# Performance work log

Hardware: AMD Instinct MI355X
Metric: run time of the kernel (lower is better)

Reference implementation:

```python
import jax, jax.numpy as jnp
import numpy as np

TEMPERATURE = 0.1
EPS = 1e-12  # F.normalize default eps


def _l2norm(x):
    n = jnp.sqrt(jnp.sum(x * x, axis=-1, keepdims=True))
    return x / jnp.maximum(n, EPS)


def setup_inputs() -> dict:
    key = jax.random.key(0)
    k1, k2, k3 = jax.random.split(key, 3)
    G, NA, NO, D = 256, 256, 512, 128
    student_nodes = jax.random.normal(k1, (G * NA, D), dtype=jnp.float32)
    teacher_nodes = jax.random.normal(k2, (G * NO, D), dtype=jnp.float32)
    # local indices into each original graph's node block (as in t_nodes_all[kept_indices])
    kept_node_indices = jax.random.randint(k3, (G * NA,), 0, NO, dtype=jnp.int64)
    return {
        "student_nodes": student_nodes,
        "teacher_nodes": teacher_nodes,
        "kept_node_indices": kept_node_indices,
        "num_graphs": G,
        "n_aug": NA,
        "n_orig": NO,
    }


def reference(student_nodes, teacher_nodes, kept_node_indices, num_graphs, n_aug, n_orig):
    D = student_nodes.shape[-1]
    # ragged batch regularized: ptr boundaries -> fixed-size reshape
    s = _l2norm(student_nodes.reshape(num_graphs, n_aug, D))      # [G, Na, D]
    t = _l2norm(teacher_nodes.reshape(num_graphs, n_orig, D))     # [G, No, D]
    kept = kept_node_indices.reshape(num_graphs, n_aug)           # [G, Na]
    t_aligned = jnp.take_along_axis(t, kept[:, :, None], axis=1)  # [G, Na, D]
    scores = jnp.einsum("gid,gjd->gij", s, t_aligned) / TEMPERATURE  # [G, Na, Na]
    logp = jax.nn.log_softmax(scores, axis=-1)
    idx = jnp.arange(n_aug)
    # CE with labels = arange: -logp[g, i, i], mean over i per graph, then mean over graphs
    per_graph_ce = -jnp.mean(logp[:, idx, idx], axis=-1)          # [G]
    return jnp.mean(per_graph_ce)
```

## Files before the change

### kernel.cpp

```cpp
#include <hip/hip_runtime.h>
#include <hip/hip_bf16.h>

using f32x4  = __attribute__((ext_vector_type(4))) float;
using bf16x8 = __attribute__((ext_vector_type(8))) short;

constexpr int   G_NUM = 256;
constexpr int   NAUG  = 256;
constexpr int   NORIG = 512;
constexpr int   DIM   = 128;
constexpr float INV_T = 10.0f;

__device__ __forceinline__ short f32_to_bf16_bits(float x) {
    unsigned u = __float_as_uint(x);
    u += 0x7fffu + ((u >> 16) & 1u);
    return (short)(u >> 16);
}

__global__ __launch_bounds__(512, 4) void nlcl_main(
    const float* __restrict__ student,
    const float* __restrict__ teacher,
    const int*   __restrict__ kept,
    float*       __restrict__ block_sums)
{
    __shared__ short t_lds[NAUG * DIM];
    __shared__ float rt_lds[NAUG];
    __shared__ float rs_lds[128];
    __shared__ float red[8];

    const int bid = blockIdx.x;
    const int logical = (bid & 7) * 64 + (bid >> 3);
    const int g    = logical >> 1;
    const int half = logical & 1;

    const int tid  = threadIdx.x;
    const int lane = tid & 63;
    const int wave = tid >> 6;
    const int rbase = half * 128;

    const float* s_base = student + (size_t)g * NAUG * DIM;
    const float* t_base = teacher + (size_t)g * NORIG * DIM;
    const int*   k_base = kept + g * NAUG;

    const int ccol  = lane & 15;
    const int cquad = lane >> 4;

    const int hw = tid >> 5;
    const int hl = tid & 31;

    int idxv[16];
    #pragma unroll
    for (int it = 0; it < 16; ++it) idxv[it] = k_base[it * 16 + hw];

    const int srow = rbase + wave * 16 + ccol;
    const float* rp = s_base + srow * DIM;
    float4 sv[8];
    #pragma unroll
    for (int kc = 0; kc < 4; ++kc) {
        sv[kc * 2]     = *reinterpret_cast<const float4*>(rp + kc * 32 + cquad * 8);
        sv[kc * 2 + 1] = *reinterpret_cast<const float4*>(rp + kc * 32 + cquad * 8 + 4);
    }

    float4 gv0[4], gv1[4];
    #pragma unroll
    for (int i = 0; i < 4; ++i)
        gv0[i] = *reinterpret_cast<const float4*>(t_base + (size_t)idxv[i] * DIM + hl * 4);
    #pragma unroll
    for (int i = 0; i < 4; ++i)
        gv1[i] = *reinterpret_cast<const float4*>(t_base + (size_t)idxv[4 + i] * DIM + hl * 4);

    bf16x8 afrag[4];
    {
        float ss = 0.f;
        #pragma unroll
        for (int kc = 0; kc < 4; ++kc) {
            const float4 a = sv[kc * 2], b = sv[kc * 2 + 1];
            afrag[kc][0] = f32_to_bf16_bits(a.x); afrag[kc][1] = f32_to_bf16_bits(a.y);
            afrag[kc][2] = f32_to_bf16_bits(a.z); afrag[kc][3] = f32_to_bf16_bits(a.w);
            afrag[kc][4] = f32_to_bf16_bits(b.x); afrag[kc][5] = f32_to_bf16_bits(b.y);
            afrag[kc][6] = f32_to_bf16_bits(b.z); afrag[kc][7] = f32_to_bf16_bits(b.w);
            ss += a.x * a.x + a.y * a.y + a.z * a.z + a.w * a.w;
            ss += b.x * b.x + b.y * b.y + b.z * b.z + b.w * b.w;
        }
        ss += __shfl_xor(ss, 16);
        ss += __shfl_xor(ss, 32);
        if (cquad == 0)
            rs_lds[wave * 16 + ccol] = rsqrtf(fmaxf(ss, 1e-24f)) * INV_T;
    }

    char* tl = reinterpret_cast<char*>(t_lds);
    #pragma unroll
    for (int c = 0; c < 4; ++c) {
        float4 cur[4];
        #pragma unroll
        for (int i = 0; i < 4; ++i) cur[i] = (c & 1) ? gv1[i] : gv0[i];
        if (c < 2) {
            #pragma unroll
            for (int i = 0; i < 4; ++i) {
                float4 nxt = *reinterpret_cast<const float4*>(
                    t_base + (size_t)idxv[(c + 2) * 4 + i] * DIM + hl * 4);
                if (c & 1) gv1[i] = nxt; else gv0[i] = nxt;
            }
        }
        #pragma unroll
        for (int i = 0; i < 4; ++i) {
            const int it = c * 4 + i;
            const int j  = it * 16 + hw;
            const float4 v = cur[i];
            short4 o;
            o.x = f32_to_bf16_bits(v.x); o.y = f32_to_bf16_bits(v.y);
            o.z = f32_to_bf16_bits(v.z); o.w = f32_to_bf16_bits(v.w);
            const int byte = j * 256 + ((hl * 8) ^ ((j & 7) << 4));
            *reinterpret_cast<short4*>(tl + byte) = o;
            float ss = v.x * v.x + v.y * v.y + v.z * v.z + v.w * v.w;
            ss += __shfl_xor(ss, 1);
            ss += __shfl_xor(ss, 2);
            ss += __shfl_xor(ss, 4);
            ss += __shfl_xor(ss, 8);
            ss += __shfl_xor(ss, 16);
            if (hl == 0)
                rt_lds[j] = rsqrtf(fmaxf(ss, 1e-24f));
        }
    }
    __syncthreads();

    float sumexp[4] = {0.f, 0.f, 0.f, 0.f};
    float diagsum = 0.f;
    const char* tlc = reinterpret_cast<const char*>(t_lds);
    float rs[4];
    #pragma unroll
    for (int reg = 0; reg < 4; ++reg)
        rs[reg] = rs_lds[wave * 16 + cquad * 4 + reg];

    for (int ct = 0; ct < 16; ++ct) {
        f32x4 acc = {0.f, 0.f, 0.f, 0.f};
        const int j = ct * 16 + ccol;
        const float rt = rt_lds[j];
        #pragma unroll
        for (int kc = 0; kc < 4; ++kc) {
            const int byte = j * 256 + (((kc * 64) + (cquad * 16)) ^ ((j & 7) << 4));
            const bf16x8 b = *reinterpret_cast<const bf16x8*>(tlc + byte);
            acc = __builtin_amdgcn_mfma_f32_16x16x32_bf16(afrag[kc], b, acc, 0, 0, 0);
        }
        #pragma unroll
        for (int reg = 0; reg < 4; ++reg) {
            const int row = rbase + wave * 16 + cquad * 4 + reg;
            const float l = acc[reg] * rs[reg] * rt;
            sumexp[reg] += __expf(l);
            if (j == row) diagsum += l;
        }
    }

    float ce = 0.f;
    #pragma unroll
    for (int reg = 0; reg < 4; ++reg) {
        float s = sumexp[reg];
        s += __shfl_xor(s, 1);
        s += __shfl_xor(s, 2);
        s += __shfl_xor(s, 4);
        s += __shfl_xor(s, 8);
        if (ccol == 0) ce += __logf(s);
    }
    ce -= diagsum;
    ce += __shfl_xor(ce, 1);
    ce += __shfl_xor(ce, 2);
    ce += __shfl_xor(ce, 4);
    ce += __shfl_xor(ce, 8);
    ce += __shfl_xor(ce, 16);
    ce += __shfl_xor(ce, 32);

    if (lane == 0) red[wave] = ce;
    __syncthreads();
    if (tid == 0) {
        float t = 0.f;
        #pragma unroll
        for (int w = 0; w < 8; ++w) t += red[w];
        block_sums[bid] = t;
    }
}

__global__ void nlcl_reduce(const float* __restrict__ block_sums,
                            float* __restrict__ out)
{
    __shared__ float r[8];
    const int tid = threadIdx.x;
    float v = block_sums[tid];
    v += __shfl_xor(v, 1);
    v += __shfl_xor(v, 2);
    v += __shfl_xor(v, 4);
    v += __shfl_xor(v, 8);
    v += __shfl_xor(v, 16);
    v += __shfl_xor(v, 32);
    if ((tid & 63) == 0) r[tid >> 6] = v;
    __syncthreads();
    if (tid == 0) {
        float t = 0.f;
        #pragma unroll
        for (int w = 0; w < 8; ++w) t += r[w];
        out[0] = t * (1.0f / ((float)G_NUM * (float)NAUG));
    }
}

extern "C" void kernel_launch(void* const* d_in, const int* in_sizes, int n_in,
                              void* d_out, int out_size, void* d_ws, size_t ws_size,
                              hipStream_t stream) {
    (void)in_sizes; (void)n_in; (void)out_size; (void)ws_size;
    const float* student = (const float*)d_in[0];
    const float* teacher = (const float*)d_in[1];
    const int*   kept    = (const int*)d_in[2];
    float* bs  = (float*)d_ws;
    float* out = (float*)d_out;

    nlcl_main<<<512, 512, 0, stream>>>(student, teacher, kept, bs);
    nlcl_reduce<<<1, 512, 0, stream>>>(bs, out);
}
```

Measured before the change: 25.13 us.

## Split teacher staging into two halves and fuse final reduction via last-block atomic

Issues all sixteen teacher row gathers up front in two register batches, stores the first half to LDS, and syncs. It then overlaps storing the second half with MFMA over the first half, separated by a second barrier. The separate reduce kernel is replaced by a last-block-done atomic counter pattern, with the counter zeroed by a memset each call. This doubles the register footprint for gathered rows, which may reduce occupancy, and trades one kernel launch for a memset plus an atomic.

```diff
diff --git a/kernel.cpp b/kernel.cpp
--- a/kernel.cpp
+++ b/kernel.cpp
@@ -4,11 +4,12 @@
 using f32x4  = __attribute__((ext_vector_type(4))) float;
 using bf16x8 = __attribute__((ext_vector_type(8))) short;
 
-constexpr int   G_NUM = 256;
-constexpr int   NAUG  = 256;
-constexpr int   NORIG = 512;
-constexpr int   DIM   = 128;
-constexpr float INV_T = 10.0f;
+constexpr int   G_NUM  = 256;
+constexpr int   NAUG   = 256;
+constexpr int   NORIG  = 512;
+constexpr int   DIM    = 128;
+constexpr float INV_T  = 10.0f;
+constexpr int   NBLK   = 512;
 
 __device__ __forceinline__ short f32_to_bf16_bits(float x) {
     unsigned u = __float_as_uint(x);
@@ -20,12 +21,15 @@
     const float* __restrict__ student,
     const float* __restrict__ teacher,
     const int*   __restrict__ kept,
-    float*       __restrict__ block_sums)
+    float*       __restrict__ block_sums,
+    unsigned*    __restrict__ counter,
+    float*       __restrict__ out)
 {
     __shared__ short t_lds[NAUG * DIM];
     __shared__ float rt_lds[NAUG];
     __shared__ float rs_lds[128];
     __shared__ float red[8];
+    __shared__ int   is_last;
 
     const int bid = blockIdx.x;
     const int logical = (bid & 7) * 64 + (bid >> 3);
@@ -60,13 +64,13 @@
         sv[kc * 2 + 1] = *reinterpret_cast<const float4*>(rp + kc * 32 + cquad * 8 + 4);
     }
 
-    float4 gv0[4], gv1[4];
-    #pragma unroll
-    for (int i = 0; i < 4; ++i)
+    float4 gv0[8], gv1[8];
+    #pragma unroll
+    for (int i = 0; i < 8; ++i)
         gv0[i] = *reinterpret_cast<const float4*>(t_base + (size_t)idxv[i] * DIM + hl * 4);
     #pragma unroll
-    for (int i = 0; i < 4; ++i)
-        gv1[i] = *reinterpret_cast<const float4*>(t_base + (size_t)idxv[4 + i] * DIM + hl * 4);
+    for (int i = 0; i < 8; ++i)
+        gv1[i] = *reinterpret_cast<const float4*>(t_base + (size_t)idxv[8 + i] * DIM + hl * 4);
 
     bf16x8 afrag[4];
     {
@@ -89,39 +93,41 @@
 
     char* tl = reinterpret_cast<char*>(t_lds);
     #pragma unroll
-    for (int c = 0; c < 4; ++c) {
-        float4 cur[4];
-        #pragma unroll
-        for (int i = 0; i < 4; ++i) cur[i] = (c & 1) ? gv1[i] : gv0[i];
-        if (c < 2) {
-            #pragma unroll
-            for (int i = 0; i < 4; ++i) {
-                float4 nxt = *reinterpret_cast<const float4*>(
-                    t_base + (size_t)idxv[(c + 2) * 4 + i] * DIM + hl * 4);
-                if (c & 1) gv1[i] = nxt; else gv0[i] = nxt;
-            }
-        }
-        #pragma unroll
-        for (int i = 0; i < 4; ++i) {
-            const int it = c * 4 + i;
-            const int j  = it * 16 + hw;
-            const float4 v = cur[i];
-            short4 o;
-            o.x = f32_to_bf16_bits(v.x); o.y = f32_to_bf16_bits(v.y);
-            o.z = f32_to_bf16_bits(v.z); o.w = f32_to_bf16_bits(v.w);
-            const int byte = j * 256 + ((hl * 8) ^ ((j & 7) << 4));
-            *reinterpret_cast<short4*>(tl + byte) = o;
-            float ss = v.x * v.x + v.y * v.y + v.z * v.z + v.w * v.w;
-            ss += __shfl_xor(ss, 1);
-            ss += __shfl_xor(ss, 2);
-            ss += __shfl_xor(ss, 4);
-            ss += __shfl_xor(ss, 8);
-            ss += __shfl_xor(ss, 16);
-            if (hl == 0)
-                rt_lds[j] = rsqrtf(fmaxf(ss, 1e-24f));
-        }
-    }
-    __syncthreads();
+    for (int i = 0; i < 8; ++i) {
+        const int j = i * 16 + hw;
+        const float4 v = gv0[i];
+        short4 o;
+        o.x = f32_to_bf16_bits(v.x); o.y = f32_to_bf16_bits(v.y);
+        o.z = f32_to_bf16_bits(v.z); o.w = f32_to_bf16_bits(v.w);
+        const int byte = j * 256 + ((hl * 8) ^ ((j & 7) << 4));
+        *reinterpret_cast<short4*>(tl + byte) = o;
+        float ss = v.x * v.x + v.y * v.y + v.z * v.z + v.w * v.w;
+        ss += __shfl_xor(ss, 1);
+        ss += __shfl_xor(ss, 2);
+        ss += __shfl_xor(ss, 4);
+        ss += __shfl_xor(ss, 8);
+        ss += __shfl_xor(ss, 16);
+        if (hl == 0) rt_lds[j] = rsqrtf(fmaxf(ss, 1e-24f));
+    }
+    __syncthreads();
+
+    #pragma unroll
+    for (int i = 0; i < 8; ++i) {
+        const int j = (8 + i) * 16 + hw;
+        const float4 v = gv1[i];
+        short4 o;
+        o.x = f32_to_bf16_bits(v.x); o.y = f32_to_bf16_bits(v.y);
+        o.z = f32_to_bf16_bits(v.z); o.w = f32_to_bf16_bits(v.w);
+        const int byte = j * 256 + ((hl * 8) ^ ((j & 7) << 4));
+        *reinterpret_cast<short4*>(tl + byte) = o;
+        float ss = v.x * v.x + v.y * v.y + v.z * v.z + v.w * v.w;
+        ss += __shfl_xor(ss, 1);
+        ss += __shfl_xor(ss, 2);
+        ss += __shfl_xor(ss, 4);
+        ss += __shfl_xor(ss, 8);
+        ss += __shfl_xor(ss, 16);
+        if (hl == 0) rt_lds[j] = rsqrtf(fmaxf(ss, 1e-24f));
+    }
 
     float sumexp[4] = {0.f, 0.f, 0.f, 0.f};
     float diagsum = 0.f;
@@ -131,7 +137,29 @@
     for (int reg = 0; reg < 4; ++reg)
         rs[reg] = rs_lds[wave * 16 + cquad * 4 + reg];
 
-    for (int ct = 0; ct < 16; ++ct) {
+    #pragma unroll 2
+    for (int ct = 0; ct < 8; ++ct) {
+        f32x4 acc = {0.f, 0.f, 0.f, 0.f};
+        const int j = ct * 16 + ccol;
+        const float rt = rt_lds[j];
+        #pragma unroll
+        for (int kc = 0; kc < 4; ++kc) {
+            const int byte = j * 256 + (((kc * 64) + (cquad * 16)) ^ ((j & 7) << 4));
+            const bf16x8 b = *reinterpret_cast<const bf16x8*>(tlc + byte);
+            acc = __builtin_amdgcn_mfma_f32_16x16x32_bf16(afrag[kc], b, acc, 0, 0, 0);
+        }
+        #pragma unroll
+        for (int reg = 0; reg < 4; ++reg) {
+            const int row = rbase + wave * 16 + cquad * 4 + reg;
+            const float l = acc[reg] * rs[reg] * rt;
+            sumexp[reg] += __expf(l);
+            if (j == row) diagsum += l;
+        }
+    }
+    __syncthreads();
+
+    #pragma unroll 2
+    for (int ct = 8; ct < 16; ++ct) {
         f32x4 acc = {0.f, 0.f, 0.f, 0.f};
         const int j = ct * 16 + ccol;
         const float rt = rt_lds[j];
@@ -175,28 +203,29 @@
         #pragma unroll
         for (int w = 0; w < 8; ++w) t += red[w];
         block_sums[bid] = t;
-    }
-}
-
-__global__ void nlcl_reduce(const float* __restrict__ block_sums,
-                            float* __restrict__ out)
-{
-    __shared__ float r[8];
-    const int tid = threadIdx.x;
-    float v = block_sums[tid];
-    v += __shfl_xor(v, 1);
-    v += __shfl_xor(v, 2);
-    v += __shfl_xor(v, 4);
-    v += __shfl_xor(v, 8);
-    v += __shfl_xor(v, 16);
-    v += __shfl_xor(v, 32);
-    if ((tid & 63) == 0) r[tid >> 6] = v;
-    __syncthreads();
-    if (tid == 0) {
-        float t = 0.f;
-        #pragma unroll
-        for (int w = 0; w < 8; ++w) t += r[w];
-        out[0] = t * (1.0f / ((float)G_NUM * (float)NAUG));
+        __threadfence();
+        const unsigned old = atomicAdd(counter, 1u);
+        is_last = (old == NBLK - 1) ? 1 : 0;
+    }
+    __syncthreads();
+
+    if (is_last) {
+        __threadfence();
+        float v = atomicAdd(&block_sums[tid], 0.0f);
+        v += __shfl_xor(v, 1);
+        v += __shfl_xor(v, 2);
+        v += __shfl_xor(v, 4);
+        v += __shfl_xor(v, 8);
+        v += __shfl_xor(v, 16);
+        v += __shfl_xor(v, 32);
+        if (lane == 0) red[wave] = v;
+        __syncthreads();
+        if (tid == 0) {
+            float t = 0.f;
+            #pragma unroll
+            for (int w = 0; w < 8; ++w) t += red[w];
+            out[0] = t * (1.0f / ((float)G_NUM * (float)NAUG));
+        }
     }
 }
 
@@ -207,9 +236,11 @@
     const float* student = (const float*)d_in[0];
     const float* teacher = (const float*)d_in[1];
     const int*   kept    = (const int*)d_in[2];
-    float* bs  = (float*)d_ws;
-    float* out = (float*)d_out;
-
-    nlcl_main<<<512, 512, 0, stream>>>(student, teacher, kept, bs);
-    nlcl_reduce<<<1, 512, 0, stream>>>(bs, out);
+
+    unsigned* counter = (unsigned*)d_ws;
+    float*    bs      = (float*)((char*)d_ws + 256);
+    float*    out     = (float*)d_out;
+
+    hipMemsetAsync(counter, 0, sizeof(unsigned), stream);
+    nlcl_main<<<NBLK, 512, 0, stream>>>(student, teacher, kept, bs, counter, out);
 }
```

New measurement: 37.12 us. 47.7% more time.
